# Kernel optimization log

Measured on AMD Instinct MI355X. Metric: run time of the kernel, lower is better.

The kernel has to match this reference:

```python
import jax, jax.numpy as jnp
import numpy as np
from jax import lax

B, C, H, W = 2, 96, 64, 64
D_INNER, D_STATE, DT_RANK, K = 192, 16, 6, 4
EPS = 1e-5


def _ln(x, g, b):
    mu = jnp.mean(x, -1, keepdims=True)
    var = jnp.var(x, -1, keepdims=True)
    return (x - mu) * lax.rsqrt(var + EPS) * g + b


def setup_inputs() -> dict:
    key = jax.random.key(0)
    ks = jax.random.split(key, 10)
    f = lambda k, s, sc=0.02: jax.random.normal(k, s, dtype=jnp.float32) * sc
    return {
        "rgb": jax.random.normal(ks[0], (B, C, H, W), dtype=jnp.float32),
        "t": jax.random.normal(ks[1], (B, C, H, W), dtype=jnp.float32),
        "conv_w": f(ks[2], (C, 2 * C, 3, 3), 0.05),
        "conv_b": jnp.zeros((C,), jnp.float32),
        "bn_gamma": jnp.ones((C,), jnp.float32),
        "bn_beta": jnp.zeros((C,), jnp.float32),
        "bn_mean": jnp.zeros((C,), jnp.float32),
        "bn_var": jnp.ones((C,), jnp.float32),
        "ln_gamma": jnp.ones((C,), jnp.float32),
        "ln_beta": jnp.zeros((C,), jnp.float32),
        "in_proj_w": f(ks[3], (2 * D_INNER, C)),
        "dwconv_w": f(ks[4], (D_INNER, 1, 3, 3), 0.1),
        "dwconv_b": jnp.zeros((D_INNER,), jnp.float32),
        "x_proj_w": f(ks[5], (K, DT_RANK + 2 * D_STATE, D_INNER)),
        "dt_w": f(ks[6], (K, D_INNER, DT_RANK), 0.1),
        "dt_b": jnp.full((K, D_INNER), float(np.log(np.expm1(0.01))), jnp.float32),
        "A_logs": jnp.log(jnp.tile(jnp.arange(1, D_STATE + 1, dtype=jnp.float32), (K * D_INNER, 1))),
        "Ds": jnp.ones((K * D_INNER,), jnp.float32),
        "out_norm_gamma": jnp.ones((D_INNER,), jnp.float32),
        "out_norm_beta": jnp.zeros((D_INNER,), jnp.float32),
        "out_proj_w": f(ks[7], (C, D_INNER)),
    }


def _forward(rgb, t, conv_w, conv_b, bn_gamma, bn_beta, bn_mean, bn_var,
             ln_gamma, ln_beta, in_proj_w, dwconv_w, dwconv_b, x_proj_w,
             dt_w, dt_b, A_logs, Ds, out_norm_gamma, out_norm_beta, out_proj_w):
    dn = ("NCHW", "OIHW", "NCHW")
    # BasicConv: conv + BN(eval) + ReLU (dropout inactive in eval)
    x = jnp.concatenate([rgb, t], axis=1)
    x = lax.conv_general_dilated(x, conv_w, (1, 1), "SAME", dimension_numbers=dn)
    x = x + conv_b[None, :, None, None]
    x = (x - bn_mean[None, :, None, None]) * lax.rsqrt(bn_var[None, :, None, None] + EPS)
    x = x * bn_gamma[None, :, None, None] + bn_beta[None, :, None, None]
    x = jax.nn.relu(x)
    # permute to (B,H,W,C) and LayerNorm over channels
    x = _ln(jnp.transpose(x, (0, 2, 3, 1)), ln_gamma, ln_beta)
    # ---- SS2D ----
    xz = jnp.einsum("bhwc,ec->bhwe", x, in_proj_w)  # e = 2*d_inner
    xc, z = jnp.split(xz, 2, axis=-1)
    xc = jnp.transpose(xc, (0, 3, 1, 2))  # (B, d_inner, H, W)
    xc = lax.conv_general_dilated(xc, dwconv_w, (1, 1), "SAME",
                                  dimension_numbers=dn, feature_group_count=D_INNER)
    xc = jax.nn.silu(xc + dwconv_b[None, :, None, None])
    L = H * W
    # cross-scan: row-major, col-major, and their reverses -> (B,4,d,L)
    x_flat = xc.reshape(B, D_INNER, L)
    x_tr = jnp.transpose(xc, (0, 1, 3, 2)).reshape(B, D_INNER, L)
    xs = jnp.stack([x_flat, x_tr], axis=1)
    xs = jnp.concatenate([xs, xs[..., ::-1]], axis=1)  # (B,K,d,L)
    x_dbl = jnp.einsum("bkdl,kcd->bkcl", xs, x_proj_w)
    dts = x_dbl[:, :, :DT_RANK]
    Bs = x_dbl[:, :, DT_RANK:DT_RANK + D_STATE]  # (B,K,N,L)
    Cs = x_dbl[:, :, DT_RANK + D_STATE:]         # (B,K,N,L)
    dts = jnp.einsum("bkrl,kdr->bkdl", dts, dt_w)
    A = -jnp.exp(A_logs).reshape(K, D_INNER, D_STATE)
    Dsk = Ds.reshape(K, D_INNER)
    delta = jax.nn.softplus(dts + dt_b[None, :, :, None])  # (B,K,d,L)
    du = delta * xs

    def step(h, inp):
        dl, dul, Bl, Cl = inp  # (B,K,d),(B,K,d),(B,K,N),(B,K,N)
        h = h * jnp.exp(dl[..., None] * A) + dul[..., None] * Bl[:, :, None, :]
        y = jnp.einsum("bkdn,bkn->bkd", h, Cl)
        return h, y

    h0 = jnp.zeros((B, K, D_INNER, D_STATE), delta.dtype)
    _, ys = lax.scan(step, h0, (
        jnp.transpose(delta, (3, 0, 1, 2)),
        jnp.transpose(du, (3, 0, 1, 2)),
        jnp.transpose(Bs, (3, 0, 1, 2)),
        jnp.transpose(Cs, (3, 0, 1, 2)),
    ))
    out_y = jnp.transpose(ys, (1, 2, 3, 0)) + xs * Dsk[None, :, :, None]  # (B,K,d,L)
    # merge four scan directions back to row-major order
    inv_y = out_y[:, 2:4, :, ::-1]
    wh_y = jnp.transpose(out_y[:, 1].reshape(B, D_INNER, W, H), (0, 1, 3, 2)).reshape(B, D_INNER, L)
    invwh_y = jnp.transpose(inv_y[:, 1].reshape(B, D_INNER, W, H), (0, 1, 3, 2)).reshape(B, D_INNER, L)
    y = out_y[:, 0] + inv_y[:, 0] + wh_y + invwh_y  # (B,d,L)
    y = jnp.transpose(y, (0, 2, 1)).reshape(B, H, W, D_INNER)
    y = _ln(y, out_norm_gamma, out_norm_beta)
    y = y * jax.nn.silu(z)
    out = jnp.einsum("bhwd,cd->bhwc", y, out_proj_w)
    return jnp.transpose(out, (0, 3, 1, 2))  # (B,C,H,W)


def reference(rgb, t, conv_w, conv_b, bn_gamma, bn_beta, bn_mean, bn_var,
              ln_gamma, ln_beta, in_proj_w, dwconv_w, dwconv_b, x_proj_w,
              dt_w, dt_b, A_logs, Ds, out_norm_gamma, out_norm_beta, out_proj_w):
    return _forward(rgb, t, conv_w, conv_b, bn_gamma, bn_beta, bn_mean, bn_var,
                    ln_gamma, ln_beta, in_proj_w, dwconv_w, dwconv_b, x_proj_w,
                    dt_w, dt_b, A_logs, Ds, out_norm_gamma, out_norm_beta, out_proj_w)
```

## Files before the change

### kernel.cpp

```cpp
#include <hip/hip_runtime.h>
#include <math.h>

#define HW 4096
#define CC 96
#define DD 192
#define NS 16
#define KK 4
#define LC 64
#define NC 64
#define NCH (8*DD*NS)

__device__ __forceinline__ float siluf(float x){ return x / (1.f + __expf(-x)); }
__device__ __forceinline__ float softplus_fast(float x){ return (x > 20.f) ? x : __logf(1.f + __expf(x)); }

__device__ __forceinline__ int lmap_xs(int k, int l){
  if (k == 1) return ((l & 63) << 6) | (l >> 6);
  if (k == 2) return (HW - 1) - l;
  if (k == 3) { int r = (HW - 1) - l; return ((r & 63) << 6) | (r >> 6); }
  return l;
}

__global__ void k_prep(const float* __restrict__ cw, const float* __restrict__ xpw,
                       float* __restrict__ wT, float* __restrict__ xpwT){
  int o = blockIdx.x*256 + threadIdx.x;
  if (o < 165888){
    int co = o % 96; int rest = o / 96; int tap = rest % 9; int cig = rest / 9;
    wT[o] = cw[((size_t)co*192 + cig)*9 + tap];
  } else if (o < 165888 + 29184){
    int o2 = o - 165888;
    int c = o2 % 38; int rest = o2 / 38; int d = rest % 192; int k = rest / 192;
    xpwT[o2] = xpw[((size_t)(k*38 + c))*192 + d];
  }
}

__global__ void __launch_bounds__(256, 4)
k_conv1(const float* __restrict__ rgb, const float* __restrict__ tt,
        const float* __restrict__ wT, float* __restrict__ pbuf){
  __shared__ float in_lds[6][6][68];
  __shared__ __align__(16) float w_lds[6][9][64];
  int bi = blockIdx.x;
  int kc  = bi & 7;         int ci0 = kc*24;
  int cog = (bi >> 3) & 1;  int co0 = cog*48;
  int b   = (bi >> 4) & 1;
  int pt  = bi >> 5;        int h0 = pt*4;
  int tid = threadIdx.x;
  int pg = tid & 31;  int r = pg >> 3;  int w0 = (pg & 7)*8;
  int cg = tid >> 5;  int co_t = cg*6;

  float acc[6][8];
  #pragma unroll
  for (int c = 0; c < 6; ++c)
    #pragma unroll
    for (int p = 0; p < 8; ++p) acc[c][p] = 0.f;

  for (int s = 0; s < 4; ++s){
    if (s) __syncthreads();
    if (tid < 72){ int side = tid & 1; int rr = (tid % 12) >> 1; int ci = tid / 12;
                   in_lds[ci][rr][side ? 65 : 0] = 0.f; }
    for (int i = tid; i < 2304; i += 256){
      int ci = i / 384; int rem = i - ci*384; int rr = rem >> 6; int w = rem & 63;
      int grow = h0 - 1 + rr;
      int cig = ci0 + s*6 + ci;
      float v = 0.f;
      if (grow >= 0 && grow < 64){
        const float* src = (cig < CC) ? (rgb + (size_t)(b*CC+cig)*HW)
                                      : (tt  + (size_t)(b*CC+cig-CC)*HW);
        v = src[grow*64 + w];
      }
      in_lds[ci][rr][w+1] = v;
    }
    for (int i = tid; i < 2592; i += 256){
      int co = i % 48; int rest = i / 48; int tap = rest % 9; int ci = rest / 9;
      w_lds[ci][tap][(co/6)*8 + (co%6)] =
          wT[((size_t)(ci0 + s*6 + ci)*9 + tap)*96 + co0 + co];
    }
    __syncthreads();
    #pragma unroll
    for (int ci = 0; ci < 6; ++ci){
      float rowv[3][10];
      #pragma unroll
      for (int rr = 0; rr < 3; ++rr){
        const float* rp = &in_lds[ci][r+rr][w0];
        float4 a = *(const float4*)rp;
        float4 bb = *(const float4*)(rp+4);
        float2 cc = *(const float2*)(rp+8);
        rowv[rr][0]=a.x; rowv[rr][1]=a.y; rowv[rr][2]=a.z; rowv[rr][3]=a.w;
        rowv[rr][4]=bb.x; rowv[rr][5]=bb.y; rowv[rr][6]=bb.z; rowv[rr][7]=bb.w;
        rowv[rr][8]=cc.x; rowv[rr][9]=cc.y;
      }
      #pragma unroll
      for (int tap = 0; tap < 9; ++tap){
        int rt = tap/3, ct = tap - rt*3;
        float4 wa = *(const float4*)&w_lds[ci][tap][cg*8];
        float2 wb = *(const float2*)&w_lds[ci][tap][cg*8+4];
        float wv[6] = {wa.x, wa.y, wa.z, wa.w, wb.x, wb.y};
        #pragma unroll
        for (int p = 0; p < 8; ++p){
          float iv = rowv[rt][p + ct];
          #pragma unroll
          for (int c = 0; c < 6; ++c) acc[c][p] += wv[c]*iv;
        }
      }
    }
  }
  #pragma unroll
  for (int p = 0; p < 8; ++p){
    int pix = (h0 + r)*64 + w0 + p;
    float* o = pbuf + (((size_t)kc*2 + b)*HW + pix)*CC + co0 + co_t;
    float2 o0 = {acc[0][p], acc[1][p]};
    float2 o1 = {acc[2][p], acc[3][p]};
    float2 o2 = {acc[4][p], acc[5][p]};
    *(float2*)&o[0] = o0; *(float2*)&o[2] = o1; *(float2*)&o[4] = o2;
  }
}

__global__ void k_convred(const float* __restrict__ pbuf, const float* __restrict__ cb,
                          const float* __restrict__ bng, const float* __restrict__ bnb,
                          const float* __restrict__ bnm, const float* __restrict__ bnv,
                          const float* __restrict__ lng, const float* __restrict__ lnb,
                          float* __restrict__ xn){
  __shared__ float sm[4], sm2[4], smu[2], srs[2];
  int tid = threadIdx.x;
  int half = tid >> 7;
  int c = tid & 127;
  int pixg = blockIdx.x*2 + half;
  int b = pixg >> 12; int pix = pixg & (HW-1);
  float v = 0.f;
  if (c < CC){
    #pragma unroll
    for (int kc = 0; kc < 8; ++kc)
      v += pbuf[(((size_t)kc*2 + b)*HW + pix)*CC + c];
    v += cb[c];
    v = (v - bnm[c]) * rsqrtf(bnv[c] + 1e-5f);
    v = v * bng[c] + bnb[c];
    v = fmaxf(v, 0.f);
  }
  float s = v, s2 = v*v;
  #pragma unroll
  for (int off = 32; off; off >>= 1){ s += __shfl_down(s, off); s2 += __shfl_down(s2, off); }
  if ((tid & 63) == 0){ sm[tid>>6] = s; sm2[tid>>6] = s2; }
  __syncthreads();
  if (tid < 2){
    float ts = sm[2*tid] + sm[2*tid+1];
    float ts2 = sm2[2*tid] + sm2[2*tid+1];
    float mu = ts * (1.f/CC);
    float var = ts2 * (1.f/CC) - mu*mu;
    smu[tid] = mu; srs[tid] = rsqrtf(var + 1e-5f);
  }
  __syncthreads();
  if (c < CC)
    xn[(size_t)pixg*CC + c] = (v - smu[half])*srs[half]*lng[c] + lnb[c];
}

__global__ void k_inproj(const float* __restrict__ xn, const float* __restrict__ ipw,
                         float* __restrict__ xz){
  __shared__ float As[64][97];
  __shared__ __align__(16) float Bs[96][68];
  int p0 = blockIdx.x*64;
  int e0 = blockIdx.y*64;
  int tid = threadIdx.x;
  for (int idx = tid; idx < 64*96; idx += 256){
    int r = idx/96, c = idx - r*96;
    As[r][c] = xn[(size_t)(p0+r)*96 + c];
  }
  for (int idx = tid; idx < 96*64; idx += 256){
    int c = idx/64, e = idx - c*64;
    Bs[c][e] = ipw[(size_t)(e0+e)*96 + c];
  }
  __syncthreads();
  int tx = tid & 15, ty = tid >> 4;
  float acc[4][4] = {};
  for (int c = 0; c < 96; ++c){
    float a[4];
    #pragma unroll
    for (int i = 0; i < 4; ++i) a[i] = As[ty*4+i][c];
    float4 bb = *(const float4*)&Bs[c][tx*4];
    float bv[4] = {bb.x, bb.y, bb.z, bb.w};
    #pragma unroll
    for (int i = 0; i < 4; ++i)
      #pragma unroll
      for (int j = 0; j < 4; ++j) acc[i][j] += a[i]*bv[j];
  }
  for (int i = 0; i < 4; ++i){
    float4 o = {acc[i][0], acc[i][1], acc[i][2], acc[i][3]};
    *(float4*)&xz[(size_t)(p0+ty*4+i)*384 + e0 + tx*4] = o;
  }
}

__global__ void k_dwconv(const float* __restrict__ xz, const float* __restrict__ dww,
                         const float* __restrict__ dwb, float* __restrict__ xc){
  int gid = blockIdx.x*256 + threadIdx.x;
  int dq = gid % 48; int bp = gid / 48;
  int d = dq*4;
  int pix = bp & (HW-1); int b = bp >> 12;
  int h = pix >> 6, w = pix & 63;
  float4 acc = *(const float4*)&dwb[d];
  float wreg[4][9];
  #pragma unroll
  for (int j = 0; j < 4; ++j)
    #pragma unroll
    for (int t = 0; t < 9; ++t) wreg[j][t] = dww[(d+j)*9 + t];
  #pragma unroll
  for (int dh = -1; dh <= 1; ++dh){
    int hh = h + dh;
    if (hh < 0 || hh > 63) continue;
    #pragma unroll
    for (int dw2 = -1; dw2 <= 1; ++dw2){
      int ww = w + dw2;
      if (ww < 0 || ww > 63) continue;
      float4 v = *(const float4*)&xz[((size_t)b*HW + hh*64 + ww)*384 + d];
      int t = (dh+1)*3 + (dw2+1);
      acc.x += v.x*wreg[0][t];
      acc.y += v.y*wreg[1][t];
      acc.z += v.z*wreg[2][t];
      acc.w += v.w*wreg[3][t];
    }
  }
  float4 o = {siluf(acc.x), siluf(acc.y), siluf(acc.z), siluf(acc.w)};
  *(float4*)&xc[(size_t)bp*DD + d] = o;
}

__global__ void __launch_bounds__(320)
k_xdbl(const float* __restrict__ xc, const float* __restrict__ xpwT,
       const float* __restrict__ dtw, const float* __restrict__ dtb,
       float* __restrict__ Bsb, float* __restrict__ Csb, float* __restrict__ dlt){
  __shared__ float xs_t[48*20];
  __shared__ float w_t[48*80];
  __shared__ float dts_s[2][16][8];
  int blk = blockIdx.x;
  int lt = blk & 255; int p = (blk >> 8) & 1; int b = blk >> 9;
  int l0 = lt*16;
  int tid = threadIdx.x;
  int lg = tid & 15, cg = tid >> 4;
  int c0 = cg*4;
  int b4kA = b*4 + p, b4kB = b*4 + p + 2;
  int wc = tid % 76;
  int wg = tid / 76;
  int kkW = (wc < 38) ? p : (p + 2);
  int ccW = (wc < 38) ? wc : wc - 38;

  float acc[4] = {0.f, 0.f, 0.f, 0.f};
  for (int ch = 0; ch < 4; ++ch){
    int d0 = ch*48;
    if (ch) __syncthreads();
    if (tid < 192){
      int j = tid & 15; int dq = tid >> 4;
      int l = l0 + j;
      int lm = (p == 0) ? l : (((l & 63) << 6) | (l >> 6));
      float4 v = *(const float4*)&xc[((size_t)b*HW + lm)*DD + d0 + dq*4];
      xs_t[(dq*4+0)*20 + j] = v.x;
      xs_t[(dq*4+1)*20 + j] = v.y;
      xs_t[(dq*4+2)*20 + j] = v.z;
      xs_t[(dq*4+3)*20 + j] = v.w;
    }
    if (wg < 4){
      #pragma unroll
      for (int dd = wg; dd < 48; dd += 4)
        w_t[dd*80 + wc] = xpwT[((size_t)kkW*192 + d0 + dd)*38 + ccW];
    }
    __syncthreads();
    #pragma unroll 4
    for (int dd = 0; dd < 48; ++dd){
      float4 wv = *(const float4*)&w_t[dd*80 + c0];
      float xv = xs_t[dd*20 + lg];
      acc[0] += wv.x*xv;
      acc[1] += wv.y*xv;
      acc[2] += wv.z*xv;
      acc[3] += wv.w*xv;
    }
  }
  {
    int lf = l0 + lg;
    int lr = HW - 1 - lf;
    #pragma unroll
    for (int j = 0; j < 4; ++j){
      int c = c0 + j;
      float v = acc[j];
      if      (c <  6) dts_s[0][lg][c] = v;
      else if (c < 22) Bsb [((size_t)b4kA*HW + lf)*NS + (c-6)]   = v;
      else if (c < 38) Csb [((size_t)b4kA*HW + lf)*NS + (c-22)]  = v;
      else if (c < 44) dts_s[1][lg][c-38] = v;
      else if (c < 60) Bsb [((size_t)b4kB*HW + lr)*NS + (c-44)]  = v;
      else if (c < 76) Csb [((size_t)b4kB*HW + lr)*NS + (c-60)]  = v;
    }
  }
  __syncthreads();

  for (int o = tid; o < 6144; o += 320){
    int dir = (o >= 3072) ? 1 : 0;
    int oo = o - dir*3072;
    int lj = oo / 192;
    int d  = oo - lj*192;
    int k  = dir ? (p + 2) : p;
    int b4k = dir ? b4kB : b4kA;
    int lout = dir ? (HW - 1 - (l0 + lj)) : (l0 + lj);
    const float* t = dts_s[dir][lj];
    const float* wp = &dtw[(size_t)(k*DD + d)*6];
    float s = dtb[k*DD + d] + t[0]*wp[0] + t[1]*wp[1] + t[2]*wp[2]
                            + t[3]*wp[3] + t[4]*wp[4] + t[5]*wp[5];
    dlt[((size_t)b4k*HW + lout)*DD + d] = softplus_fast(s);
  }
}

__global__ void k_scan1(const float* __restrict__ dlt, const float* __restrict__ xc,
                        const float* __restrict__ Bsb, const float* __restrict__ Alog,
                        float* __restrict__ Ac, float* __restrict__ Bc){
  int tid = blockIdx.x*256 + threadIdx.x;
  int ng = tid & 3;
  int t2 = tid >> 2;
  int d = t2 % DD;
  int rest = t2 / DD;
  int chunk = rest & (NC-1);
  int b4k = rest >> 6;
  int k = b4k & 3, b = b4k >> 2;
  float4 Af = *(const float4*)&Alog[(size_t)(k*DD+d)*NS + ng*4];
  float Av[4] = {-__expf(Af.x), -__expf(Af.y), -__expf(Af.z), -__expf(Af.w)};
  float h[4] = {0.f,0.f,0.f,0.f};
  float ap[4] = {1.f,1.f,1.f,1.f};
  int l0 = chunk*LC;
  const float* dp  = dlt + ((size_t)b4k*HW + l0)*DD + d;
  const float4* Bp4 = (const float4*)(Bsb + ((size_t)b4k*HW + l0)*NS) + ng;
  const float* xcb = xc + (size_t)b*HW*DD + d;
  float dvc = dp[0];
  float xvc = xcb[(size_t)lmap_xs(k, l0)*DD];
  float4 Bvc = Bp4[0];
  #pragma unroll 4
  for (int i = 0; i < LC; ++i){
    float dvn = 0.f, xvn = 0.f; float4 Bvn = {0.f,0.f,0.f,0.f};
    if (i+1 < LC){
      dvn = dp[(size_t)(i+1)*DD];
      xvn = xcb[(size_t)lmap_xs(k, l0+i+1)*DD];
      Bvn = Bp4[(size_t)(i+1)*4];
    }
    float du = dvc*xvc;
    float a0 = __expf(dvc*Av[0]), a1 = __expf(dvc*Av[1]),
          a2 = __expf(dvc*Av[2]), a3 = __expf(dvc*Av[3]);
    h[0] = h[0]*a0 + du*Bvc.x; ap[0] *= a0;
    h[1] = h[1]*a1 + du*Bvc.y; ap[1] *= a1;
    h[2] = h[2]*a2 + du*Bvc.z; ap[2] *= a2;
    h[3] = h[3]*a3 + du*Bvc.w; ap[3] *= a3;
    dvc = dvn; xvc = xvn; Bvc = Bvn;
  }
  size_t base = (size_t)chunk*NCH + (size_t)(b4k*DD + d)*NS + ng*4;
  *(float4*)&Ac[base] = make_float4(ap[0],ap[1],ap[2],ap[3]);
  *(float4*)&Bc[base] = make_float4(h[0],h[1],h[2],h[3]);
}

__global__ void k_scan2(float* __restrict__ Ac, const float* __restrict__ Bc){
  int chain = blockIdx.x*256 + threadIdx.x;
  float h = 0.f;
  for (int c = 0; c < NC; ++c){
    size_t idx = (size_t)c*NCH + chain;
    float a = Ac[idx], bv = Bc[idx];
    Ac[idx] = h;
    h = a*h + bv;
  }
}

__global__ void k_scan3(const float* __restrict__ dlt, const float* __restrict__ xc,
                        const float* __restrict__ Bsb, const float* __restrict__ Csb,
                        const float* __restrict__ Alog, const float* __restrict__ hst,
                        float* __restrict__ ys){
  int tid = blockIdx.x*256 + threadIdx.x;
  int ng = tid & 3;
  int t2 = tid >> 2;
  int d = t2 % DD;
  int rest = t2 / DD;
  int chunk = rest & (NC-1);
  int b4k = rest >> 6;
  int k = b4k & 3, b = b4k >> 2;
  float4 Af = *(const float4*)&Alog[(size_t)(k*DD+d)*NS + ng*4];
  float Av[4] = {-__expf(Af.x), -__expf(Af.y), -__expf(Af.z), -__expf(Af.w)};
  size_t hbase = (size_t)chunk*NCH + (size_t)(b4k*DD + d)*NS + ng*4;
  float4 hf = *(const float4*)&hst[hbase];
  float h[4] = {hf.x, hf.y, hf.z, hf.w};
  int l0 = chunk*LC;
  const float* dp  = dlt + ((size_t)b4k*HW + l0)*DD + d;
  const float4* Bp4 = (const float4*)(Bsb + ((size_t)b4k*HW + l0)*NS) + ng;
  const float4* Cp4 = (const float4*)(Csb + ((size_t)b4k*HW + l0)*NS) + ng;
  const float* xcb = xc + (size_t)b*HW*DD + d;
  float* yp = ys + ((size_t)b4k*HW + l0)*DD + d;
  float dvc = dp[0];
  float xvc = xcb[(size_t)lmap_xs(k, l0)*DD];
  float4 Bvc = Bp4[0];
  float4 Cvc = Cp4[0];
  #pragma unroll 4
  for (int i = 0; i < LC; ++i){
    float dvn = 0.f, xvn = 0.f; float4 Bvn = {0.f,0.f,0.f,0.f}, Cvn = {0.f,0.f,0.f,0.f};
    if (i+1 < LC){
      dvn = dp[(size_t)(i+1)*DD];
      xvn = xcb[(size_t)lmap_xs(k, l0+i+1)*DD];
      Bvn = Bp4[(size_t)(i+1)*4];
      Cvn = Cp4[(size_t)(i+1)*4];
    }
    float du = dvc*xvc;
    float a0 = __expf(dvc*Av[0]), a1 = __expf(dvc*Av[1]),
          a2 = __expf(dvc*Av[2]), a3 = __expf(dvc*Av[3]);
    h[0] = h[0]*a0 + du*Bvc.x;
    h[1] = h[1]*a1 + du*Bvc.y;
    h[2] = h[2]*a2 + du*Bvc.z;
    h[3] = h[3]*a3 + du*Bvc.w;
    float y = h[0]*Cvc.x + h[1]*Cvc.y + h[2]*Cvc.z + h[3]*Cvc.w;
    y += __shfl_xor(y, 1, 4);
    y += __shfl_xor(y, 2, 4);
    if (ng == 0) yp[(size_t)i*DD] = y;
    dvc = dvn; xvc = xvn; Bvc = Bvn; Cvc = Cvn;
  }
}

__global__ void k_gate(const float* __restrict__ ys, const float* __restrict__ xc,
                       const float* __restrict__ Ds, const float* __restrict__ xz,
                       const float* __restrict__ ong, const float* __restrict__ onb,
                       float* __restrict__ yg){
  int gt = blockIdx.x*256 + threadIdx.x;
  int wave = gt >> 6;
  int lane = gt & 63;
  int b = wave >> 12; int l = wave & (HW-1);
  int l1 = ((l & 63) << 6) | (l >> 6);
  size_t base = (size_t)b*KK*HW*DD;
  float v[3]; float s = 0.f, s2 = 0.f;
  #pragma unroll
  for (int j = 0; j < 3; ++j){
    int d = lane + j*64;
    float t;
    t  = ys[base + ((size_t)0*HW + l        )*DD + d];
    t += ys[base + ((size_t)1*HW + l1       )*DD + d];
    t += ys[base + ((size_t)2*HW + (HW-1-l ))*DD + d];
    t += ys[base + ((size_t)3*HW + (HW-1-l1))*DD + d];
    t += xc[((size_t)b*HW + l)*DD + d] * (Ds[d] + Ds[DD+d] + Ds[2*DD+d] + Ds[3*DD+d]);
    v[j] = t; s += t; s2 += t*t;
  }
  #pragma unroll
  for (int off = 32; off; off >>= 1){ s += __shfl_xor(s, off); s2 += __shfl_xor(s2, off); }
  float mu = s*(1.f/DD);
  float rstd = rsqrtf(s2*(1.f/DD) - mu*mu + 1e-5f);
  #pragma unroll
  for (int j = 0; j < 3; ++j){
    int d = lane + j*64;
    float z = xz[((size_t)b*HW + l)*384 + DD + d];
    float x = (v[j]-mu)*rstd*ong[d] + onb[d];
    yg[(size_t)wave*DD + d] = x * siluf(z);
  }
}

__global__ void k_outproj(const float* __restrict__ yg, const float* __restrict__ opw,
                          float* __restrict__ out){
  __shared__ float yl[48][36];
  __shared__ float wl[48][97];
  int blk = blockIdx.x;
  int b = blk >> 7; int pt = blk & 127;
  int px0 = pt*32;
  int tid = threadIdx.x;
  int pxg = tid & 7;
  int cgi = tid >> 3;
  float acc[4][3] = {};
  for (int k0 = 0; k0 < DD; k0 += 48){
    if (k0) __syncthreads();
    for (int i = tid; i < 32*48; i += 256){
      int r = i/48, k = i - r*48;
      yl[k][r] = yg[((size_t)b*HW + px0 + r)*DD + k0 + k];
    }
    for (int i = tid; i < 96*48; i += 256){
      int c = i/48, k = i - c*48;
      wl[k][c] = opw[(size_t)c*DD + k0 + k];
    }
    __syncthreads();
    #pragma unroll 4
    for (int k = 0; k < 48; ++k){
      float4 yv = *(const float4*)&yl[k][pxg*4];
      float w0 = wl[k][cgi*3], w1 = wl[k][cgi*3+1], w2 = wl[k][cgi*3+2];
      acc[0][0] += yv.x*w0; acc[0][1] += yv.x*w1; acc[0][2] += yv.x*w2;
      acc[1][0] += yv.y*w0; acc[1][1] += yv.y*w1; acc[1][2] += yv.y*w2;
      acc[2][0] += yv.z*w0; acc[2][1] += yv.z*w1; acc[2][2] += yv.z*w2;
      acc[3][0] += yv.w*w0; acc[3][1] += yv.w*w1; acc[3][2] += yv.w*w2;
    }
  }
  #pragma unroll
  for (int j = 0; j < 3; ++j){
    int c = cgi*3 + j;
    float4 o = {acc[0][j], acc[1][j], acc[2][j], acc[3][j]};
    *(float4*)&out[((size_t)b*CC + c)*HW + px0 + pxg*4] = o;
  }
}

extern "C" void kernel_launch(void* const* d_in, const int* in_sizes, int n_in,
                              void* d_out, int out_size, void* d_ws, size_t ws_size,
                              hipStream_t stream) {
  const float* rgb   = (const float*)d_in[0];
  const float* tt    = (const float*)d_in[1];
  const float* cw    = (const float*)d_in[2];
  const float* cb    = (const float*)d_in[3];
  const float* bng   = (const float*)d_in[4];
  const float* bnb   = (const float*)d_in[5];
  const float* bnm   = (const float*)d_in[6];
  const float* bnv   = (const float*)d_in[7];
  const float* lng   = (const float*)d_in[8];
  const float* lnb   = (const float*)d_in[9];
  const float* ipw   = (const float*)d_in[10];
  const float* dww   = (const float*)d_in[11];
  const float* dwb   = (const float*)d_in[12];
  const float* xpw   = (const float*)d_in[13];
  const float* dtw   = (const float*)d_in[14];
  const float* dtb   = (const float*)d_in[15];
  const float* Alog  = (const float*)d_in[16];
  const float* Ds    = (const float*)d_in[17];
  const float* ong   = (const float*)d_in[18];
  const float* onb   = (const float*)d_in[19];
  const float* opw   = (const float*)d_in[20];
  float* out = (float*)d_out;

  float* ws = (float*)d_ws;
  float* xn   = ws + 786432;
  float* xz   = ws + 1572864;
  float* xc   = ws + 4718592;
  float* Bsb  = ws + 6291456;
  float* Csb  = ws + 6815744;
  float* dlt  = ws + 7340032;
  float* ysb  = ws + 13631488;
  float* pbuf = ws + 1572864;
  float* Ac   = ws;
  float* Bc   = ysb;
  float* yg   = ws + 7340032;
  float* wT   = ws + 16777216;
  float* xpwT = ws + 16943104;

  k_prep<<<762, 256, 0, stream>>>(cw, xpw, wT, xpwT);
  k_conv1<<<512, 256, 0, stream>>>(rgb, tt, wT, pbuf);
  k_convred<<<4096, 256, 0, stream>>>(pbuf, cb, bng, bnb, bnm, bnv, lng, lnb, xn);
  dim3 g2(128, 6);
  k_inproj<<<g2, 256, 0, stream>>>(xn, ipw, xz);
  k_dwconv<<<1536, 256, 0, stream>>>(xz, dww, dwb, xc);
  k_xdbl<<<1024, 320, 0, stream>>>(xc, xpwT, dtw, dtb, Bsb, Csb, dlt);
  k_scan1<<<1536, 256, 0, stream>>>(dlt, xc, Bsb, Alog, Ac, Bc);
  k_scan2<<<96, 256, 0, stream>>>(Ac, Bc);
  k_scan3<<<1536, 256, 0, stream>>>(dlt, xc, Bsb, Csb, Alog, Ac, ysb);
  k_gate<<<2048, 256, 0, stream>>>(ysb, xc, Ds, xz, ong, onb, yg);
  k_outproj<<<256, 256, 0, stream>>>(yg, opw, out);
}
```

Baseline: 235.1 us.

## Store delta in fp16 and deepen scan prefetch to two steps

The softplus delta buffer written by k_xdbl is now stored as half precision, which halves its write traffic and the reads by both scan kernels. The scan loops also prefetch operands two iterations ahead instead of one, to hide more global load latency. The gate output buffer is moved to a new workspace offset so it does not overlap the smaller delta buffer. Delta loses precision, which could affect accuracy over long recurrences.

```diff
diff --git a/kernel.cpp b/kernel.cpp
--- a/kernel.cpp
+++ b/kernel.cpp
@@ -1,4 +1,5 @@
 #include <hip/hip_runtime.h>
+#include <hip/hip_fp16.h>
 #include <math.h>
 
 #define HW 4096
@@ -223,7 +224,7 @@
 __global__ void __launch_bounds__(320)
 k_xdbl(const float* __restrict__ xc, const float* __restrict__ xpwT,
        const float* __restrict__ dtw, const float* __restrict__ dtb,
-       float* __restrict__ Bsb, float* __restrict__ Csb, float* __restrict__ dlt){
+       float* __restrict__ Bsb, float* __restrict__ Csb, __half* __restrict__ dlt){
   __shared__ float xs_t[48*20];
   __shared__ float w_t[48*80];
   __shared__ float dts_s[2][16][8];
@@ -298,11 +299,11 @@
     const float* wp = &dtw[(size_t)(k*DD + d)*6];
     float s = dtb[k*DD + d] + t[0]*wp[0] + t[1]*wp[1] + t[2]*wp[2]
                             + t[3]*wp[3] + t[4]*wp[4] + t[5]*wp[5];
-    dlt[((size_t)b4k*HW + lout)*DD + d] = softplus_fast(s);
-  }
-}
-
-__global__ void k_scan1(const float* __restrict__ dlt, const float* __restrict__ xc,
+    dlt[((size_t)b4k*HW + lout)*DD + d] = __float2half(softplus_fast(s));
+  }
+}
+
+__global__ void k_scan1(const __half* __restrict__ dlt, const float* __restrict__ xc,
                         const float* __restrict__ Bsb, const float* __restrict__ Alog,
                         float* __restrict__ Ac, float* __restrict__ Bc){
   int tid = blockIdx.x*256 + threadIdx.x;
@@ -318,28 +319,32 @@
   float h[4] = {0.f,0.f,0.f,0.f};
   float ap[4] = {1.f,1.f,1.f,1.f};
   int l0 = chunk*LC;
-  const float* dp  = dlt + ((size_t)b4k*HW + l0)*DD + d;
+  const __half* dp = dlt + ((size_t)b4k*HW + l0)*DD + d;
   const float4* Bp4 = (const float4*)(Bsb + ((size_t)b4k*HW + l0)*NS) + ng;
   const float* xcb = xc + (size_t)b*HW*DD + d;
-  float dvc = dp[0];
-  float xvc = xcb[(size_t)lmap_xs(k, l0)*DD];
-  float4 Bvc = Bp4[0];
+  float dv0 = __half2float(dp[0]);
+  float xv0 = xcb[(size_t)lmap_xs(k, l0)*DD];
+  float4 Bv0 = Bp4[0];
+  float dv1 = __half2float(dp[DD]);
+  float xv1 = xcb[(size_t)lmap_xs(k, l0+1)*DD];
+  float4 Bv1 = Bp4[4];
   #pragma unroll 4
   for (int i = 0; i < LC; ++i){
-    float dvn = 0.f, xvn = 0.f; float4 Bvn = {0.f,0.f,0.f,0.f};
-    if (i+1 < LC){
-      dvn = dp[(size_t)(i+1)*DD];
-      xvn = xcb[(size_t)lmap_xs(k, l0+i+1)*DD];
-      Bvn = Bp4[(size_t)(i+1)*4];
-    }
-    float du = dvc*xvc;
-    float a0 = __expf(dvc*Av[0]), a1 = __expf(dvc*Av[1]),
-          a2 = __expf(dvc*Av[2]), a3 = __expf(dvc*Av[3]);
-    h[0] = h[0]*a0 + du*Bvc.x; ap[0] *= a0;
-    h[1] = h[1]*a1 + du*Bvc.y; ap[1] *= a1;
-    h[2] = h[2]*a2 + du*Bvc.z; ap[2] *= a2;
-    h[3] = h[3]*a3 + du*Bvc.w; ap[3] *= a3;
-    dvc = dvn; xvc = xvn; Bvc = Bvn;
+    float dv2 = 0.f, xv2 = 0.f; float4 Bv2 = {0.f,0.f,0.f,0.f};
+    if (i+2 < LC){
+      dv2 = __half2float(dp[(size_t)(i+2)*DD]);
+      xv2 = xcb[(size_t)lmap_xs(k, l0+i+2)*DD];
+      Bv2 = Bp4[(size_t)(i+2)*4];
+    }
+    float du = dv0*xv0;
+    float a0 = __expf(dv0*Av[0]), a1 = __expf(dv0*Av[1]),
+          a2 = __expf(dv0*Av[2]), a3 = __expf(dv0*Av[3]);
+    h[0] = h[0]*a0 + du*Bv0.x; ap[0] *= a0;
+    h[1] = h[1]*a1 + du*Bv0.y; ap[1] *= a1;
+    h[2] = h[2]*a2 + du*Bv0.z; ap[2] *= a2;
+    h[3] = h[3]*a3 + du*Bv0.w; ap[3] *= a3;
+    dv0 = dv1; xv0 = xv1; Bv0 = Bv1;
+    dv1 = dv2; xv1 = xv2; Bv1 = Bv2;
   }
   size_t base = (size_t)chunk*NCH + (size_t)(b4k*DD + d)*NS + ng*4;
   *(float4*)&Ac[base] = make_float4(ap[0],ap[1],ap[2],ap[3]);
@@ -357,7 +362,7 @@
   }
 }
 
-__global__ void k_scan3(const float* __restrict__ dlt, const float* __restrict__ xc,
+__global__ void k_scan3(const __half* __restrict__ dlt, const float* __restrict__ xc,
                         const float* __restrict__ Bsb, const float* __restrict__ Csb,
                         const float* __restrict__ Alog, const float* __restrict__ hst,
                         float* __restrict__ ys){
@@ -375,36 +380,41 @@
   float4 hf = *(const float4*)&hst[hbase];
   float h[4] = {hf.x, hf.y, hf.z, hf.w};
   int l0 = chunk*LC;
-  const float* dp  = dlt + ((size_t)b4k*HW + l0)*DD + d;
+  const __half* dp = dlt + ((size_t)b4k*HW + l0)*DD + d;
   const float4* Bp4 = (const float4*)(Bsb + ((size_t)b4k*HW + l0)*NS) + ng;
   const float4* Cp4 = (const float4*)(Csb + ((size_t)b4k*HW + l0)*NS) + ng;
   const float* xcb = xc + (size_t)b*HW*DD + d;
   float* yp = ys + ((size_t)b4k*HW + l0)*DD + d;
-  float dvc = dp[0];
-  float xvc = xcb[(size_t)lmap_xs(k, l0)*DD];
-  float4 Bvc = Bp4[0];
-  float4 Cvc = Cp4[0];
+  float dv0 = __half2float(dp[0]);
+  float xv0 = xcb[(size_t)lmap_xs(k, l0)*DD];
+  float4 Bv0 = Bp4[0];
+  float4 Cv0 = Cp4[0];
+  float dv1 = __half2float(dp[DD]);
+  float xv1 = xcb[(size_t)lmap_xs(k, l0+1)*DD];
+  float4 Bv1 = Bp4[4];
+  float4 Cv1 = Cp4[4];
   #pragma unroll 4
   for (int i = 0; i < LC; ++i){
-    float dvn = 0.f, xvn = 0.f; float4 Bvn = {0.f,0.f,0.f,0.f}, Cvn = {0.f,0.f,0.f,0.f};
-    if (i+1 < LC){
-      dvn = dp[(size_t)(i+1)*DD];
-      xvn = xcb[(size_t)lmap_xs(k, l0+i+1)*DD];
-      Bvn = Bp4[(size_t)(i+1)*4];
-      Cvn = Cp4[(size_t)(i+1)*4];
-    }
-    float du = dvc*xvc;
-    float a0 = __expf(dvc*Av[0]), a1 = __expf(dvc*Av[1]),
-          a2 = __expf(dvc*Av[2]), a3 = __expf(dvc*Av[3]);
-    h[0] = h[0]*a0 + du*Bvc.x;
-    h[1] = h[1]*a1 + du*Bvc.y;
-    h[2] = h[2]*a2 + du*Bvc.z;
-    h[3] = h[3]*a3 + du*Bvc.w;
-    float y = h[0]*Cvc.x + h[1]*Cvc.y + h[2]*Cvc.z + h[3]*Cvc.w;
+    float dv2 = 0.f, xv2 = 0.f; float4 Bv2 = {0.f,0.f,0.f,0.f}, Cv2 = {0.f,0.f,0.f,0.f};
+    if (i+2 < LC){
+      dv2 = __half2float(dp[(size_t)(i+2)*DD]);
+      xv2 = xcb[(size_t)lmap_xs(k, l0+i+2)*DD];
+      Bv2 = Bp4[(size_t)(i+2)*4];
+      Cv2 = Cp4[(size_t)(i+2)*4];
+    }
+    float du = dv0*xv0;
+    float a0 = __expf(dv0*Av[0]), a1 = __expf(dv0*Av[1]),
+          a2 = __expf(dv0*Av[2]), a3 = __expf(dv0*Av[3]);
+    h[0] = h[0]*a0 + du*Bv0.x;
+    h[1] = h[1]*a1 + du*Bv0.y;
+    h[2] = h[2]*a2 + du*Bv0.z;
+    h[3] = h[3]*a3 + du*Bv0.w;
+    float y = h[0]*Cv0.x + h[1]*Cv0.y + h[2]*Cv0.z + h[3]*Cv0.w;
     y += __shfl_xor(y, 1, 4);
     y += __shfl_xor(y, 2, 4);
     if (ng == 0) yp[(size_t)i*DD] = y;
-    dvc = dvn; xvc = xvn; Bvc = Bvn; Cvc = Cvn;
+    dv0 = dv1; xv0 = xv1; Bv0 = Bv1; Cv0 = Cv1;
+    dv1 = dv2; xv1 = xv2; Bv1 = Bv2; Cv1 = Cv2;
   }
 }
 
@@ -515,12 +525,12 @@
   float* xc   = ws + 4718592;
   float* Bsb  = ws + 6291456;
   float* Csb  = ws + 6815744;
-  float* dlt  = ws + 7340032;
+  __half* dlt = (__half*)(ws + 7340032);
   float* ysb  = ws + 13631488;
   float* pbuf = ws + 1572864;
   float* Ac   = ws;
   float* Bc   = ysb;
-  float* yg   = ws + 7340032;
+  float* yg   = ws + 10485760;
   float* wT   = ws + 16777216;
   float* xpwT = ws + 16943104;
 
```

Result: slower. 241.3 us (+2.6%).
